# Kernel optimization log

Hardware: AMD Instinct MI355X
Metric: run time of the kernel (lower is better)

## Reference

```python
import jax, jax.numpy as jnp
import numpy as np

VOCAB, D_MODEL, RANK = 128000, 2048, 16
B, S = 4, 4096

def setup_inputs() -> dict:
    key = jax.random.key(0)
    k1, k2, k3, k4 = jax.random.split(key, 4)
    x = jax.random.randint(k1, (B, S), 0, VOCAB, dtype=jnp.int64)
    base_weight = jax.random.normal(k2, (VOCAB, D_MODEL), dtype=jnp.float32) * 0.02
    lora_A = jax.random.normal(k3, (RANK, VOCAB), dtype=jnp.float32) * 0.02
    lora_B = jax.random.normal(k4, (D_MODEL, RANK), dtype=jnp.float32) * 0.02
    return {"x": x, "base_weight": base_weight, "lora_A": lora_A, "lora_B": lora_B}

def reference(x, base_weight, lora_A, lora_B):
    # base embedding gather: [B,S,D]
    base_out = base_weight[x]
    # LoRA: gather rows of A^T (per-token low-rank code) then thin GEMM with B^T
    ar = lora_A.T[x]                              # [B,S,r]
    lora_out = jnp.einsum('bsr,dr->bsd', ar, lora_B)  # [B,S,D]
    return base_out + lora_out
```

## Files before the change

kernel.cpp:

```cpp
#include <hip/hip_runtime.h>


#define VOCAB   128000
#define DMODEL  2048
#define RANK    16
#define TPB     32
#define THREADS 1024
#define PF      4

typedef float fx4 __attribute__((ext_vector_type(4)));
typedef float fx2 __attribute__((ext_vector_type(2)));

__global__ __launch_bounds__(THREADS, 8)
void embed_lora_kernel(const int* __restrict__ x,
                       const float* __restrict__ W,
                       const float* __restrict__ A,
                       const float* __restrict__ Bm,
                       float* __restrict__ out) {
    __shared__ fx4 code4[TPB][RANK / 4];

    const int tid   = threadIdx.x;
    const int tbase = blockIdx.x * TPB;

    if (tid < 512) {
        const int j   = tid >> 4;
        const int r   = tid & 15;
        const int tok = x[tbase + j];
        ((float*)&code4[j][0])[r] = A[(size_t)r * VOCAB + (size_t)tok];
    }

    const int d0 = tid * 2;
    fx4 B0[4], B1[4];
    {
        const fx4* Bp = (const fx4*)(Bm + (size_t)d0 * RANK);
        #pragma unroll
        for (int q = 0; q < 4; ++q) {
            B0[q] = Bp[q];
            B1[q] = Bp[4 + q];
        }
    }

    fx2 wbuf[PF];
    #pragma unroll
    for (int p = 0; p < PF; ++p) {
        const size_t row = (size_t)x[tbase + p] * DMODEL;
        wbuf[p] = __builtin_nontemporal_load(&((const fx2*)(W + row))[tid]);
    }

    __syncthreads();

    #pragma unroll
    for (int j = 0; j < TPB; ++j) {
        const fx2 w = wbuf[j % PF];
        if (j + PF < TPB) {
            const size_t row = (size_t)x[tbase + j + PF] * DMODEL;
            wbuf[j % PF] = __builtin_nontemporal_load(&((const fx2*)(W + row))[tid]);
        }

        const fx4 c0 = code4[j][0];
        const fx4 c1 = code4[j][1];
        const fx4 c2 = code4[j][2];
        const fx4 c3 = code4[j][3];

        float s0, s1;
        s0  = B0[0].x * c0.x + B0[0].y * c0.y + B0[0].z * c0.z + B0[0].w * c0.w;
        s0 += B0[1].x * c1.x + B0[1].y * c1.y + B0[1].z * c1.z + B0[1].w * c1.w;
        s0 += B0[2].x * c2.x + B0[2].y * c2.y + B0[2].z * c2.z + B0[2].w * c2.w;
        s0 += B0[3].x * c3.x + B0[3].y * c3.y + B0[3].z * c3.z + B0[3].w * c3.w;

        s1  = B1[0].x * c0.x + B1[0].y * c0.y + B1[0].z * c0.z + B1[0].w * c0.w;
        s1 += B1[1].x * c1.x + B1[1].y * c1.y + B1[1].z * c1.z + B1[1].w * c1.w;
        s1 += B1[2].x * c2.x + B1[2].y * c2.y + B1[2].z * c2.z + B1[2].w * c2.w;
        s1 += B1[3].x * c3.x + B1[3].y * c3.y + B1[3].z * c3.z + B1[3].w * c3.w;

        fx2 o;
        o.x = w.x + s0;
        o.y = w.y + s1;

        __builtin_nontemporal_store(o, &((fx2*)out)[(size_t)(tbase + j) * (DMODEL / 2) + tid]);
    }
}

extern "C" void kernel_launch(void* const* d_in, const int* in_sizes, int n_in,
                              void* d_out, int out_size, void* d_ws, size_t ws_size,
                              hipStream_t stream) {
    const int*   x  = (const int*)d_in[0];
    const float* W  = (const float*)d_in[1];
    const float* A  = (const float*)d_in[2];
    const float* Bm = (const float*)d_in[3];
    float*       o  = (float*)d_out;

    const int n_tokens = in_sizes[0];
    const int n_blocks = n_tokens / TPB;

    embed_lora_kernel<<<n_blocks, THREADS, 0, stream>>>(x, W, A, Bm, o);
}
```

Measured before the change: 62.08 us.

## Split LoRA code gather into a separate pre-pass kernel using workspace

Adds a small kernel that gathers the per-token rank-16 LoRA codes from A into a contiguous workspace buffer. The main kernel then loads those codes with vectorized coalesced reads instead of doing scattered strided loads of A at the start of every block. The goal is to take the strided gather latency off the critical path of the main embedding kernel. The cost is an extra kernel launch and a round trip through the workspace. The old in-kernel gather remains as a fallback when the workspace is too small.

Result: slower. 80.37 us (+29.5%).

```diff
diff --git a/kernel.cpp b/kernel.cpp
--- a/kernel.cpp
+++ b/kernel.cpp
@@ -11,10 +11,23 @@
 typedef float fx4 __attribute__((ext_vector_type(4)));
 typedef float fx2 __attribute__((ext_vector_type(2)));
 
+__global__ __launch_bounds__(256)
+void gather_codes_kernel(const int* __restrict__ x,
+                         const float* __restrict__ A,
+                         float* __restrict__ codes, int n16) {
+    const int gid = blockIdx.x * 256 + threadIdx.x;
+    if (gid < n16) {
+        const int t = gid >> 4;
+        const int r = gid & 15;
+        codes[gid] = A[(size_t)r * VOCAB + (size_t)x[t]];
+    }
+}
+
+template <bool GATHER>
 __global__ __launch_bounds__(THREADS, 8)
 void embed_lora_kernel(const int* __restrict__ x,
                        const float* __restrict__ W,
-                       const float* __restrict__ A,
+                       const float* __restrict__ A_or_codes,
                        const float* __restrict__ Bm,
                        float* __restrict__ out) {
     __shared__ fx4 code4[TPB][RANK / 4];
@@ -22,11 +35,18 @@
     const int tid   = threadIdx.x;
     const int tbase = blockIdx.x * TPB;
 
-    if (tid < 512) {
-        const int j   = tid >> 4;
-        const int r   = tid & 15;
-        const int tok = x[tbase + j];
-        ((float*)&code4[j][0])[r] = A[(size_t)r * VOCAB + (size_t)tok];
+    if (GATHER) {
+        if (tid < TPB * RANK) {
+            const int j   = tid >> 4;
+            const int r   = tid & 15;
+            const int tok = x[tbase + j];
+            ((float*)&code4[0][0])[tid] = A_or_codes[(size_t)r * VOCAB + (size_t)tok];
+        }
+    } else {
+        if (tid < TPB * RANK / 4) {
+            ((fx4*)&code4[0][0])[tid] =
+                ((const fx4*)(A_or_codes + (size_t)tbase * RANK))[tid];
+        }
     }
 
     const int d0 = tid * 2;
@@ -92,6 +112,13 @@
 
     const int n_tokens = in_sizes[0];
     const int n_blocks = n_tokens / TPB;
+    const int n16      = n_tokens * RANK;
 
-    embed_lora_kernel<<<n_blocks, THREADS, 0, stream>>>(x, W, A, Bm, o);
+    if (ws_size >= (size_t)n16 * sizeof(float)) {
+        float* codes = (float*)d_ws;
+        gather_codes_kernel<<<(n16 + 255) / 256, 256, 0, stream>>>(x, A, codes, n16);
+        embed_lora_kernel<false><<<n_blocks, THREADS, 0, stream>>>(x, W, codes, Bm, o);
+    } else {
+        embed_lora_kernel<true><<<n_blocks, THREADS, 0, stream>>>(x, W, A, Bm, o);
+    }
 }
```

## Split LoRA code gather into two halves overlapped with embedding streaming

Applied to the files above, without the earlier changes.

The block's 32-token LoRA code gather is split into two 16-token halves in double-buffered shared memory. The second half's A loads are issued before the first half is processed and only written to shared memory just before they are needed. The full __syncthreads is replaced by a barrier that waits only on LDS counters, so the outstanding global W prefetches are not drained at the barrier. This is meant to hide the scattered A-gather latency behind the base-weight streaming, at the cost of a second barrier and more code.

Result: slower. 64.69 us (+4.2%).

```diff
diff --git a/kernel.cpp b/kernel.cpp
--- a/kernel.cpp
+++ b/kernel.cpp
@@ -5,11 +5,18 @@
 #define DMODEL  2048
 #define RANK    16
 #define TPB     32
+#define HALF    16
 #define THREADS 1024
 #define PF      4
 
 typedef float fx4 __attribute__((ext_vector_type(4)));
 typedef float fx2 __attribute__((ext_vector_type(2)));
+
+__device__ __forceinline__ void barrier_nodrain() {
+    asm volatile("s_waitcnt lgkmcnt(0)" ::: "memory");
+    __builtin_amdgcn_s_barrier();
+    __builtin_amdgcn_sched_barrier(0);
+}
 
 __global__ __launch_bounds__(THREADS, 8)
 void embed_lora_kernel(const int* __restrict__ x,
@@ -17,16 +24,22 @@
                        const float* __restrict__ A,
                        const float* __restrict__ Bm,
                        float* __restrict__ out) {
-    __shared__ fx4 code4[TPB][RANK / 4];
+    __shared__ fx4 code4[2][HALF][RANK / 4];
 
     const int tid   = threadIdx.x;
     const int tbase = blockIdx.x * TPB;
+    const bool gth  = (tid < HALF * RANK);
+    const int  gj   = tid >> 4;
+    const int  gr   = tid & 15;
 
-    if (tid < 512) {
-        const int j   = tid >> 4;
-        const int r   = tid & 15;
-        const int tok = x[tbase + j];
-        ((float*)&code4[j][0])[r] = A[(size_t)r * VOCAB + (size_t)tok];
+    float c0r = 0.f;
+    if (gth) c0r = A[(size_t)gr * VOCAB + (size_t)x[tbase + gj]];
+
+    fx2 wbuf[PF];
+    #pragma unroll
+    for (int p = 0; p < PF; ++p) {
+        const size_t row = (size_t)x[tbase + p] * DMODEL;
+        wbuf[p] = __builtin_nontemporal_load(&((const fx2*)(W + row))[tid]);
     }
 
     const int d0 = tid * 2;
@@ -40,43 +53,64 @@
         }
     }
 
-    fx2 wbuf[PF];
-    #pragma unroll
-    for (int p = 0; p < PF; ++p) {
-        const size_t row = (size_t)x[tbase + p] * DMODEL;
-        wbuf[p] = __builtin_nontemporal_load(&((const fx2*)(W + row))[tid]);
-    }
+    if (gth) ((float*)&code4[0][gj][0])[gr] = c0r;
+    barrier_nodrain();
 
-    __syncthreads();
+    float c1r = 0.f;
+    if (gth) c1r = A[(size_t)gr * VOCAB + (size_t)x[tbase + HALF + gj]];
 
     #pragma unroll
-    for (int j = 0; j < TPB; ++j) {
+    for (int j = 0; j < HALF; ++j) {
         const fx2 w = wbuf[j % PF];
-        if (j + PF < TPB) {
+        {
             const size_t row = (size_t)x[tbase + j + PF] * DMODEL;
             wbuf[j % PF] = __builtin_nontemporal_load(&((const fx2*)(W + row))[tid]);
         }
-
-        const fx4 c0 = code4[j][0];
-        const fx4 c1 = code4[j][1];
-        const fx4 c2 = code4[j][2];
-        const fx4 c3 = code4[j][3];
+        const fx4 c0 = code4[0][j][0];
+        const fx4 c1 = code4[0][j][1];
+        const fx4 c2 = code4[0][j][2];
+        const fx4 c3 = code4[0][j][3];
 
         float s0, s1;
         s0  = B0[0].x * c0.x + B0[0].y * c0.y + B0[0].z * c0.z + B0[0].w * c0.w;
         s0 += B0[1].x * c1.x + B0[1].y * c1.y + B0[1].z * c1.z + B0[1].w * c1.w;
         s0 += B0[2].x * c2.x + B0[2].y * c2.y + B0[2].z * c2.z + B0[2].w * c2.w;
         s0 += B0[3].x * c3.x + B0[3].y * c3.y + B0[3].z * c3.z + B0[3].w * c3.w;
-
         s1  = B1[0].x * c0.x + B1[0].y * c0.y + B1[0].z * c0.z + B1[0].w * c0.w;
         s1 += B1[1].x * c1.x + B1[1].y * c1.y + B1[1].z * c1.z + B1[1].w * c1.w;
         s1 += B1[2].x * c2.x + B1[2].y * c2.y + B1[2].z * c2.z + B1[2].w * c2.w;
         s1 += B1[3].x * c3.x + B1[3].y * c3.y + B1[3].z * c3.z + B1[3].w * c3.w;
 
-        fx2 o;
-        o.x = w.x + s0;
-        o.y = w.y + s1;
+        fx2 o; o.x = w.x + s0; o.y = w.y + s1;
+        __builtin_nontemporal_store(o, &((fx2*)out)[(size_t)(tbase + j) * (DMODEL / 2) + tid]);
+    }
 
+    if (gth) ((float*)&code4[1][gj][0])[gr] = c1r;
+    barrier_nodrain();
+
+    #pragma unroll
+    for (int j = HALF; j < TPB; ++j) {
+        const fx2 w = wbuf[j % PF];
+        if (j + PF < TPB) {
+            const size_t row = (size_t)x[tbase + j + PF] * DMODEL;
+            wbuf[j % PF] = __builtin_nontemporal_load(&((const fx2*)(W + row))[tid]);
+        }
+        const fx4 c0 = code4[1][j - HALF][0];
+        const fx4 c1 = code4[1][j - HALF][1];
+        const fx4 c2 = code4[1][j - HALF][2];
+        const fx4 c3 = code4[1][j - HALF][3];
+
+        float s0, s1;
+        s0  = B0[0].x * c0.x + B0[0].y * c0.y + B0[0].z * c0.z + B0[0].w * c0.w;
+        s0 += B0[1].x * c1.x + B0[1].y * c1.y + B0[1].z * c1.z + B0[1].w * c1.w;
+        s0 += B0[2].x * c2.x + B0[2].y * c2.y + B0[2].z * c2.z + B0[2].w * c2.w;
+        s0 += B0[3].x * c3.x + B0[3].y * c3.y + B0[3].z * c3.z + B0[3].w * c3.w;
+        s1  = B1[0].x * c0.x + B1[0].y * c0.y + B1[0].z * c0.z + B1[0].w * c0.w;
+        s1 += B1[1].x * c1.x + B1[1].y * c1.y + B1[1].z * c1.z + B1[1].w * c1.w;
+        s1 += B1[2].x * c2.x + B1[2].y * c2.y + B1[2].z * c2.z + B1[2].w * c2.w;
+        s1 += B1[3].x * c3.x + B1[3].y * c3.y + B1[3].z * c3.z + B1[3].w * c3.w;
+
+        fx2 o; o.x = w.x + s0; o.y = w.y + s1;
         __builtin_nontemporal_store(o, &((fx2*)out)[(size_t)(tbase + j) * (DMODEL / 2) + tid]);
     }
 }
```
